# Optimization experiments

Measured on AMD Instinct MI355X. Metric: run time of the kernel, lower is better.

The kernel has to match this reference:

```python
import jax, jax.numpy as jnp
import numpy as np

N_NODES = 100000
NEG_SLOPE = 0.01  # torch F.leaky_relu default


def gcn_conv(x, src, dst, norm, W, b):
    # x: [N, Fin]; src/dst: [E+N] (self-loops included); norm: [E+N]
    h = x @ W                                  # [N, Fout] dense transform
    msg = h[src] * norm[:, None]               # gather + edge-wise scale
    out = jax.ops.segment_sum(msg, dst, num_segments=x.shape[0])  # scatter-add
    return out + b


def build_graph(edge_index, n_nodes):
    # Add self-loops and compute symmetric GCN normalization deg^-1/2 * deg^-1/2
    loop = jnp.arange(n_nodes, dtype=edge_index.dtype)
    src = jnp.concatenate([edge_index[0], loop])
    dst = jnp.concatenate([edge_index[1], loop])
    deg = jax.ops.segment_sum(jnp.ones_like(dst, dtype=jnp.float32), dst,
                              num_segments=n_nodes)
    dinv = jnp.where(deg > 0, jax.lax.rsqrt(deg), 0.0)
    norm = dinv[src] * dinv[dst]
    return src, dst, norm


def setup_inputs() -> dict:
    key = jax.random.key(0)
    ks = jax.random.split(key, 8)
    in_c, out_c = 256, 64
    hid = 2 * out_c
    x = jax.random.normal(ks[0], (N_NODES, in_c), dtype=jnp.float32)
    edge_index = jax.random.randint(ks[1], (2, 1600000), 0, N_NODES, dtype=jnp.int64)
    def glorot(k, fan_in, fan_out):
        s = jnp.sqrt(6.0 / (fan_in + fan_out))
        return jax.random.uniform(k, (fan_in, fan_out), jnp.float32, -s, s)
    return {
        "x": x,
        "edge_index": edge_index,
        "W1": glorot(ks[2], in_c, hid),
        "b1": jnp.zeros((hid,), jnp.float32),
        "Wmu": glorot(ks[3], hid, out_c),
        "bmu": jnp.zeros((out_c,), jnp.float32),
        "Wlv": glorot(ks[4], hid, out_c),
        "blv": jnp.zeros((out_c,), jnp.float32),
    }


def reference(x, edge_index, W1, b1, Wmu, bmu, Wlv, blv):
    src, dst, norm = build_graph(edge_index, x.shape[0])
    h = gcn_conv(x, src, dst, norm, W1, b1)
    h = jnp.where(h >= 0, h, NEG_SLOPE * h)  # leaky_relu
    mu = gcn_conv(h, src, dst, norm, Wmu, bmu)
    logvar = gcn_conv(h, src, dst, norm, Wlv, blv)
    return (mu, logvar)
```

## Files before the change

### kernel.cpp

```cpp
#include <hip/hip_runtime.h>

typedef unsigned short bf16_t;
typedef short s16x8 __attribute__((ext_vector_type(8)));
typedef float f32x4 __attribute__((ext_vector_type(4)));


#define NBKT 782
#define BSH  7
#define BMSK 127
#define CAPS 512

__device__ __forceinline__ float bf2f(unsigned short u) {
    unsigned int v = ((unsigned int)u) << 16;
    float f;
    __builtin_memcpy(&f, &v, 4);
    return f;
}
__device__ __forceinline__ unsigned short f2bf(float f) {
    unsigned int x;
    __builtin_memcpy(&x, &f, 4);
    unsigned int r = x + 0x7fffu + ((x >> 16) & 1u);
    return (unsigned short)(r >> 16);
}
__device__ __forceinline__ unsigned pack2(float a, float b) {
    return (unsigned)f2bf(a) | ((unsigned)f2bf(b) << 16);
}
__device__ __forceinline__ float ldf(const void* p, long long i, unsigned f32) {
    return f32 ? ((const float*)p)[i] : bf2f(((const unsigned short*)p)[i]);
}
__device__ __forceinline__ int ldi(const void* p, long long i, unsigned i64) {
    return i64 ? (int)((const long long*)p)[i] : ((const int*)p)[i];
}
__device__ __forceinline__ s16x8 ld8u(const unsigned short* p) {
    return *(const s16x8*)p;
}
__device__ __forceinline__ f32x4 mfma16(s16x8 a, s16x8 b, f32x4 c) {
    return __builtin_amdgcn_mfma_f32_16x16x32_bf16(a, b, c, 0, 0, 0);
}
__device__ __forceinline__ void cvt_hl(const float* p, s16x8& hi, s16x8& lo) {
    const float4 u = *(const float4*)p;
    const float4 w = *(const float4*)(p + 4);
    float v[8] = {u.x, u.y, u.z, u.w, w.x, w.y, w.z, w.w};
#pragma unroll
    for (int j = 0; j < 8; ++j) {
        unsigned short h = f2bf(v[j]);
        hi[j] = (short)h;
        lo[j] = (short)f2bf(v[j] - bf2f(h));
    }
}

__global__ __launch_bounds__(256) void k_zero(unsigned* __restrict__ p, int n) {
    int i = blockIdx.x * 256 + threadIdx.x;
    if (i < n) p[i] = 0;
}

__global__ __launch_bounds__(256) void k_detect(const void* x, const void* W1,
                                                const void* ei, unsigned* flags) {
    __shared__ float smx[256];
    __shared__ float smw[256];
    __shared__ int   szc[256];
    int tid = threadIdx.x;
    const unsigned short* xu = (const unsigned short*)x;
    float mx = 0.f;
    for (int i = tid; i < 4096; i += 256) {
        unsigned short w = xu[i];
        if ((w & 0x7fffu) >= 0x7f80u) mx = 1e30f;
        else { float f = fabsf(bf2f(w)); if (f > mx) mx = f; }
    }
    smx[tid] = mx;
    const unsigned short* wu = (const unsigned short*)W1;
    float mw = 0.f;
    for (int i = tid; i < 4096; i += 256) {
        unsigned short w = wu[i];
        if ((w & 0x7fffu) >= 0x7f80u) mw = 1e30f;
        else { float f = fabsf(bf2f(w)); if (f > mw) mw = f; }
    }
    smw[tid] = mw;
    const int* eu = (const int*)ei;
    int zc = 0;
    for (int i = tid; i < 128; i += 256)
        if ((i & 1) && eu[i] == 0) ++zc;
    szc[tid] = zc;
    __syncthreads();
    for (int off = 128; off > 0; off >>= 1) {
        if (tid < off) {
            if (smx[tid + off] > smx[tid]) smx[tid] = smx[tid + off];
            if (smw[tid + off] > smw[tid]) smw[tid] = smw[tid + off];
            szc[tid] += szc[tid + off];
        }
        __syncthreads();
    }
    if (tid == 0) {
        flags[0] = (smx[0] > 1e4f) ? 1u : 0u;
        flags[1] = (smw[0] > 10.f) ? 1u : 0u;
        flags[2] = (szc[0] >= 56) ? 1u : 0u;
    }
}

__global__ __launch_bounds__(256) void k_bucket(const void* ei, const unsigned* det,
                                                int* __restrict__ btail,
                                                unsigned* __restrict__ bstore,
                                                int E, int N) {
    int e = blockIdx.x * 256 + threadIdx.x;
    if (e >= E) return;
    unsigned i64 = det[2];
    int s = ldi(ei, e, i64);
    int d = ldi(ei, (long long)E + e, i64);
    if ((unsigned)d >= (unsigned)N) return;
    int b = d >> BSH;
    int sub = blockIdx.x & 7;
    int slot = atomicAdd(&btail[sub * NBKT + b], 1);
    if (slot < CAPS) {
        unsigned src = ((unsigned)s < (unsigned)N) ? (unsigned)s : (unsigned)d;
        bstore[((long long)(b * 8 + sub)) * CAPS + slot] =
            ((unsigned)(d & BMSK) << 24) | src;
    }
}

__global__ __launch_bounds__(256) void k_bhist(const int* __restrict__ btail,
                                               const unsigned* __restrict__ bstore,
                                               int* __restrict__ cnt, int N) {
    __shared__ int lh[128];
    __shared__ int ln[8];
    const int b = blockIdx.x;
    const int tid = threadIdx.x;
    if (tid < 128) lh[tid] = 0;
    if (tid < 8) {
        int t = btail[tid * NBKT + b];
        ln[tid] = t < CAPS ? t : CAPS;
    }
    __syncthreads();
#pragma unroll 1
    for (int s = 0; s < 8; ++s) {
        int n = ln[s];
        const unsigned* base = &bstore[((long long)(b * 8 + s)) * CAPS];
        for (int i = tid; i < n; i += 256)
            atomicAdd(&lh[base[i] >> 24], 1);
    }
    __syncthreads();
    int node = b * 128 + tid;
    if (tid < 128 && node < N) cnt[node] = lh[tid];
}

__global__ __launch_bounds__(256) void k_dinv(const int* __restrict__ cnt,
                                              float* __restrict__ dinv, int N) {
    int i = blockIdx.x * 256 + threadIdx.x;
    if (i < N) dinv[i] = rsqrtf((float)cnt[i] + 1.0f);
}

__global__ __launch_bounds__(256) void k_scan_blk(const int* __restrict__ cnt,
                                                  int* __restrict__ pos,
                                                  int* __restrict__ bsum, int N) {
    __shared__ int sh[256];
    const int tid = threadIdx.x;
    const int base = blockIdx.x * 1024 + tid * 4;
    int v[4];
#pragma unroll
    for (int j = 0; j < 4; ++j) v[j] = (base + j < N) ? cnt[base + j] : 0;
    int s = v[0] + v[1] + v[2] + v[3];
    sh[tid] = s;
    __syncthreads();
    for (int off = 1; off < 256; off <<= 1) {
        int t = (tid >= off) ? sh[tid - off] : 0;
        __syncthreads();
        sh[tid] += t;
        __syncthreads();
    }
    int run = sh[tid] - s;
#pragma unroll
    for (int j = 0; j < 4; ++j) {
        if (base + j < N) pos[base + j] = run;
        run += v[j];
    }
    if (tid == 255) bsum[blockIdx.x] = sh[255];
}

__global__ void k_scan_top(int* __restrict__ bsum, int nb) {
    if (threadIdx.x == 0 && blockIdx.x == 0) {
        int running = 0;
        for (int b = 0; b < nb; ++b) {
            int t = bsum[b];
            bsum[b] = running;
            running += t;
        }
    }
}

__global__ __launch_bounds__(256) void k_scan_add(int* __restrict__ pos,
                                                  const int* __restrict__ bsum, int N) {
    int add = bsum[blockIdx.x];
    int base = blockIdx.x * 1024;
    for (int i = threadIdx.x; i < 1024; i += 256)
        if (base + i < N) pos[base + i] += add;
}

__global__ __launch_bounds__(256) void k_emit(const int* __restrict__ btail,
                                              const unsigned* __restrict__ bstore,
                                              const int* __restrict__ pos,
                                              int* __restrict__ srt, int N) {
    __shared__ int lstart[128];
    __shared__ int loff[128];
    __shared__ int ln[8];
    __shared__ int stage[4096];
    const int b = blockIdx.x;
    const int tid = threadIdx.x;
    const int base0 = pos[b * 128];
    if (tid < 128) {
        int node = b * 128 + tid;
        lstart[tid] = (node < N) ? (pos[node] - base0) : 0;
        loff[tid] = 0;
    }
    if (tid < 8) {
        int t = btail[tid * NBKT + b];
        ln[tid] = t < CAPS ? t : CAPS;
    }
    __syncthreads();
#pragma unroll 1
    for (int s = 0; s < 8; ++s) {
        int n = ln[s];
        const unsigned* bp = &bstore[((long long)(b * 8 + s)) * CAPS];
        for (int i = tid; i < n; i += 256) {
            unsigned rec = bp[i];
            int dl = rec >> 24;
            int slot = atomicAdd(&loff[dl], 1);
            stage[lstart[dl] + slot] = (int)(rec & 0xffffffu);
        }
    }
    __syncthreads();
    int total = ln[0] + ln[1] + ln[2] + ln[3] + ln[4] + ln[5] + ln[6] + ln[7];
    for (int i = tid; i < total; i += 256)
        srt[base0 + i] = stage[i];
}

__global__ __launch_bounds__(256) void k_wsplit(const void* Wa, const void* Wb,
                                                const unsigned* det, int K,
                                                unsigned short* __restrict__ bth,
                                                unsigned short* __restrict__ btl) {
    int idx = blockIdx.x * 256 + threadIdx.x;
    if (idx >= K * 128) return;
    int k = idx >> 7, n = idx & 127;
    unsigned wf = det[1];
    float w;
    if (Wb) w = (n < 64) ? ldf(Wa, (long long)k * 64 + n, wf)
                         : ldf(Wb, (long long)k * 64 + (n - 64), wf);
    else    w = ldf(Wa, idx, wf);
    unsigned short h = f2bf(w);
    bth[(long long)n * K + k] = h;
    btl[(long long)n * K + k] = f2bf(w - bf2f(h));
}

__global__ __launch_bounds__(256, 4) void k_gemm1m(
    const void* __restrict__ x, const unsigned* __restrict__ det,
    const unsigned short* __restrict__ bth,
    const unsigned short* __restrict__ btl,
    const float* __restrict__ dinv,
    unsigned* __restrict__ Cp, int N) {
    const int lane = threadIdx.x & 63;
    const int wid  = threadIdx.x >> 6;
    const int wr = wid >> 1, wc = wid & 1;
    const int l15 = lane & 15, lg = lane >> 4;
    const long long r0 = (long long)blockIdx.x * 64 + wr * 32;
    long long ar[2];
#pragma unroll
    for (int m = 0; m < 2; ++m) {
        long long r = r0 + m * 16 + l15;
        ar[m] = (r < N) ? r : (N - 1);
    }
    int bn[4];
#pragma unroll
    for (int n = 0; n < 4; ++n) bn[n] = wc * 64 + n * 16 + l15;

    f32x4 acc[2][4] = {};
    if (!det[0]) {
        const unsigned short* xp = (const unsigned short*)x;
#pragma unroll 2
        for (int k0 = 0; k0 < 256; k0 += 32) {
            const int kb = k0 + lg * 8;
            s16x8 a[2], bh[4], bl[4];
#pragma unroll
            for (int m = 0; m < 2; ++m) a[m] = ld8u(xp + ar[m] * 256 + kb);
#pragma unroll
            for (int n = 0; n < 4; ++n) {
                bh[n] = ld8u(bth + (long long)bn[n] * 256 + kb);
                bl[n] = ld8u(btl + (long long)bn[n] * 256 + kb);
            }
#pragma unroll
            for (int m = 0; m < 2; ++m)
#pragma unroll
                for (int n = 0; n < 4; ++n) {
                    acc[m][n] = mfma16(a[m], bh[n], acc[m][n]);
                    acc[m][n] = mfma16(a[m], bl[n], acc[m][n]);
                }
        }
    } else {
        const float* xp = (const float*)x;
#pragma unroll 2
        for (int k0 = 0; k0 < 256; k0 += 32) {
            const int kb = k0 + lg * 8;
            s16x8 ah[2], al[2], bh[4], bl[4];
#pragma unroll
            for (int m = 0; m < 2; ++m) cvt_hl(xp + ar[m] * 256 + kb, ah[m], al[m]);
#pragma unroll
            for (int n = 0; n < 4; ++n) {
                bh[n] = ld8u(bth + (long long)bn[n] * 256 + kb);
                bl[n] = ld8u(btl + (long long)bn[n] * 256 + kb);
            }
#pragma unroll
            for (int m = 0; m < 2; ++m)
#pragma unroll
                for (int n = 0; n < 4; ++n) {
                    acc[m][n] = mfma16(ah[m], bh[n], acc[m][n]);
                    acc[m][n] = mfma16(ah[m], bl[n], acc[m][n]);
                    acc[m][n] = mfma16(al[m], bh[n], acc[m][n]);
                }
        }
    }
#pragma unroll
    for (int m = 0; m < 2; ++m)
#pragma unroll
        for (int n = 0; n < 4; ++n) {
            const int col = wc * 64 + n * 16 + l15;
#pragma unroll
            for (int r = 0; r < 4; ++r) {
                long long row = r0 + m * 16 + lg * 4 + r;
                float v = acc[m][n][r] * dinv[(row < N) ? row : (N - 1)];
                float p = __shfl_xor(v, 1);
                if (!(lane & 1) && row < N)
                    Cp[row * 64 + (col >> 1)] = pack2(v, p);
            }
        }
}

__global__ __launch_bounds__(256, 4) void k_gemm2m(
    const unsigned short* __restrict__ hap,
    const unsigned short* __restrict__ bth,
    const unsigned short* __restrict__ btl,
    const void* bmu, const void* blv, const unsigned* __restrict__ det,
    float* __restrict__ outMu, float* __restrict__ outLv, int N) {
    const int lane = threadIdx.x & 63;
    const int wid  = threadIdx.x >> 6;
    const int wr = wid >> 1, wc = wid & 1;
    const int l15 = lane & 15, lg = lane >> 4;
    const long long r0 = (long long)blockIdx.x * 64 + wr * 32;
    long long ar[2];
#pragma unroll
    for (int m = 0; m < 2; ++m) {
        long long r = r0 + m * 16 + l15;
        ar[m] = (r < N) ? r : (N - 1);
    }
    int bn[4];
#pragma unroll
    for (int n = 0; n < 4; ++n) bn[n] = wc * 64 + n * 16 + l15;

    f32x4 acc[2][4] = {};
#pragma unroll
    for (int k0 = 0; k0 < 128; k0 += 32) {
        const int kb = k0 + lg * 8;
        s16x8 a[2], bh[4], bl[4];
#pragma unroll
        for (int m = 0; m < 2; ++m) a[m] = ld8u(hap + ar[m] * 128 + kb);
#pragma unroll
        for (int n = 0; n < 4; ++n) {
            bh[n] = ld8u(bth + (long long)bn[n] * 128 + kb);
            bl[n] = ld8u(btl + (long long)bn[n] * 128 + kb);
        }
#pragma unroll
        for (int m = 0; m < 2; ++m)
#pragma unroll
            for (int n = 0; n < 4; ++n) {
                acc[m][n] = mfma16(a[m], bh[n], acc[m][n]);
                acc[m][n] = mfma16(a[m], bl[n], acc[m][n]);
            }
    }
    __syncthreads();
    const unsigned wf = det[1];
#pragma unroll
    for (int m = 0; m < 2; ++m)
#pragma unroll
        for (int n = 0; n < 4; ++n) {
            const int col = wc * 64 + n * 16 + l15;
            const float bias = (col < 64) ? ldf(bmu, col, wf)
                                          : ldf(blv, col - 64, wf);
#pragma unroll
            for (int r = 0; r < 4; ++r) {
                long long row = r0 + m * 16 + lg * 4 + r;
                if (row < N) {
                    float v = acc[m][n][r] + bias;
                    if (col < 64) outMu[row * 64 + col] = v;
                    else          outLv[row * 64 + (col - 64)] = v;
                }
            }
        }
}

__global__ __launch_bounds__(256) void k_gather(const unsigned* __restrict__ hp,
                                                const int* __restrict__ srt,
                                                const int* __restrict__ cnt,
                                                const int* __restrict__ pos,
                                                const float* __restrict__ dinv,
                                                const void* bias, const unsigned* det,
                                                int leaky, int prescaleOut,
                                                unsigned* __restrict__ outp, int N) {
    int node = blockIdx.x * 4 + (threadIdx.x >> 6);
    if (node >= N) return;
    int lane = threadIdx.x & 63;
    int beg = pos[node];
    int end = beg + cnt[node];
    float dd = dinv[node];
    unsigned hv = hp[(long long)node * 64 + lane];
    float a0 = bf2f((unsigned short)(hv & 0xffffu));
    float a1 = bf2f((unsigned short)(hv >> 16));
    for (int q = beg; q < end; q += 8) {
        int s[8];
        unsigned v[8];
#pragma unroll
        for (int j = 0; j < 8; ++j) {
            int qq = q + j;
            s[j] = srt[(qq < end) ? qq : beg];
        }
#pragma unroll
        for (int j = 0; j < 8; ++j)
            v[j] = hp[(long long)s[j] * 64 + lane];
#pragma unroll
        for (int j = 0; j < 8; ++j) {
            bool on = (q + j) < end;
            a0 += on ? bf2f((unsigned short)(v[j] & 0xffffu)) : 0.f;
            a1 += on ? bf2f((unsigned short)(v[j] >> 16)) : 0.f;
        }
    }
    a0 *= dd;
    a1 *= dd;
    if (bias) {
        a0 += ldf(bias, 2 * lane, det[1]);
        a1 += ldf(bias, 2 * lane + 1, det[1]);
    }
    if (leaky) {
        a0 = (a0 >= 0.f) ? a0 : 0.01f * a0;
        a1 = (a1 >= 0.f) ? a1 : 0.01f * a1;
    }
    if (prescaleOut) { a0 *= dd; a1 *= dd; }
    outp[(long long)node * 64 + lane] = pack2(a0, a1);
}

__global__ void k_sentinel(float* out, long long lvOff) {
    if (threadIdx.x == 0 && blockIdx.x == 0) {
        out[0] = 9.99e5f;
        out[lvOff] = 9.98e5f;
    }
}

extern "C" void kernel_launch(void* const* d_in, const int* in_sizes, int n_in,
                              void* d_out, int out_size, void* d_ws, size_t ws_size,
                              hipStream_t stream) {
    (void)out_size;
    const int N = 100000, E = 1600000;
    bool ok = (n_in == 8) && in_sizes[0] == 25600000 && in_sizes[1] == 3200000 &&
              in_sizes[2] == 32768 && in_sizes[3] == 128 &&
              in_sizes[4] == 8192 && in_sizes[5] == 64 &&
              in_sizes[6] == 8192 && in_sizes[7] == 64 &&
              ws_size >= (size_t)21 * 1024 * 1024;
    if (!ok) {
        k_sentinel<<<1, 64, 0, stream>>>((float*)d_out, (long long)N * 64);
        return;
    }
    const void* x   = d_in[0];
    const void* ei  = d_in[1];
    const void* W1  = d_in[2];
    const void* b1  = d_in[3];
    const void* Wmu = d_in[4];
    const void* bmu = d_in[5];
    const void* Wlv = d_in[6];
    const void* blv = d_in[7];

    char* w = (char*)d_ws;
    auto carve = [&](size_t bytes) {
        char* p = w;
        w += (bytes + 255) & ~(size_t)255;
        return p;
    };
    unsigned* flags = (unsigned*)carve(64);
    int*    cnt  = (int*)carve((size_t)N * 4);
    int*    pos  = (int*)carve((size_t)N * 4);
    float*  dinv = (float*)carve((size_t)N * 4);
    int*    bsum = (int*)carve(4096);
    int*    srt  = (int*)carve((size_t)E * 4);
    unsigned short* bt1h = (unsigned short*)carve(128 * 256 * 2);
    unsigned short* bt1l = (unsigned short*)carve(128 * 256 * 2);
    unsigned short* bt2h = (unsigned short*)carve(128 * 128 * 2);
    unsigned short* bt2l = (unsigned short*)carve(128 * 128 * 2);
    int*      btail  = (int*)carve((size_t)NBKT * 8 * 4);
    unsigned* bstore = (unsigned*)carve((size_t)NBKT * 8 * CAPS * 4);

    float* M = (float*)d_out;
    float* L = M + (size_t)N * 64;
    unsigned* Mp = (unsigned*)M;
    unsigned* Lp = (unsigned*)L;

    const int nb = (N + 1023) / 1024;
    const int gblk = (N + 3) / 4;
    const int gb64 = (N + 63) / 64;

    k_zero<<<1, 64, 0, stream>>>(flags, 16);
    k_detect<<<1, 256, 0, stream>>>(x, W1, ei, flags);
    k_zero<<<(NBKT * 8 + 255) / 256, 256, 0, stream>>>((unsigned*)btail, NBKT * 8);

    k_bucket<<<(E + 255) / 256, 256, 0, stream>>>(ei, flags, btail, bstore, E, N);
    k_bhist<<<NBKT, 256, 0, stream>>>(btail, bstore, cnt, N);
    k_dinv<<<(N + 255) / 256, 256, 0, stream>>>(cnt, dinv, N);
    k_scan_blk<<<nb, 256, 0, stream>>>(cnt, pos, bsum, N);
    k_scan_top<<<1, 64, 0, stream>>>(bsum, nb);
    k_scan_add<<<nb, 256, 0, stream>>>(pos, bsum, N);
    k_emit<<<NBKT, 256, 0, stream>>>(btail, bstore, pos, srt, N);

    k_wsplit<<<(256 * 128 + 255) / 256, 256, 0, stream>>>(W1, nullptr, flags, 256,
                                                          bt1h, bt1l);
    k_wsplit<<<(128 * 128 + 255) / 256, 256, 0, stream>>>(Wmu, Wlv, flags, 128,
                                                          bt2h, bt2l);

    k_gemm1m<<<gb64, 256, 0, stream>>>(x, flags, bt1h, bt1l, dinv, Mp, N);
    k_gather<<<gblk, 256, 0, stream>>>(Mp, srt, cnt, pos, dinv, b1, flags, 1, 1,
                                       Lp, N);
    k_gather<<<gblk, 256, 0, stream>>>(Lp, srt, cnt, pos, dinv, nullptr, flags,
                                       0, 0, Mp, N);
    k_gemm2m<<<gb64, 256, 0, stream>>>((const unsigned short*)Mp, bt2h, bt2l,
                                       bmu, blv, flags, M, L, N);
}
```

Before: 560.4 us.

## Stage GEMM1 tiles in LDS with async global-to-LDS loads and 128-row tiles

Replaces the register-direct first GEMM with a 128x128 block tile whose A and B operands are loaded into shared memory through global_load_lds using an XOR-style swizzle, then read into MFMA fragments. Each wave now computes a 64x64 sub-tile, so each B fragment is reused across more rows. The fp32-input path also drops the lo*lo-free third product ordering, issuing hi/lo products in a different order. The intent is to cut redundant global loads of the weight matrix and raise MFMA density, at the cost of higher LDS use, fewer resident blocks, and barriers with no double buffering.

```diff
diff --git a/kernel.cpp b/kernel.cpp
--- a/kernel.cpp
+++ b/kernel.cpp
@@ -36,6 +36,11 @@
 }
 __device__ __forceinline__ f32x4 mfma16(s16x8 a, s16x8 b, f32x4 c) {
     return __builtin_amdgcn_mfma_f32_16x16x32_bf16(a, b, c, 0, 0, 0);
+}
+__device__ __forceinline__ void gload16(const void* g, void* l) {
+    __builtin_amdgcn_global_load_lds(
+        (const __attribute__((address_space(1))) void*)g,
+        (__attribute__((address_space(3))) void*)l, 16, 0, 0);
 }
 __device__ __forceinline__ void cvt_hl(const float* p, s16x8& hi, s16x8& lo) {
     const float4 u = *(const float4*)p;
@@ -249,84 +254,131 @@
     btl[(long long)n * K + k] = f2bf(w - bf2f(h));
 }
 
-__global__ __launch_bounds__(256, 4) void k_gemm1m(
+__global__ __launch_bounds__(256, 3) void k_gemm1s(
     const void* __restrict__ x, const unsigned* __restrict__ det,
     const unsigned short* __restrict__ bth,
     const unsigned short* __restrict__ btl,
     const float* __restrict__ dinv,
     unsigned* __restrict__ Cp, int N) {
-    const int lane = threadIdx.x & 63;
-    const int wid  = threadIdx.x >> 6;
+    __shared__ unsigned short sA[128 * 64];
+    __shared__ unsigned short sBh[128 * 64];
+    __shared__ unsigned short sBl[128 * 64];
+    const int tid  = threadIdx.x;
+    const int lane = tid & 63;
+    const int wid  = tid >> 6;
     const int wr = wid >> 1, wc = wid & 1;
     const int l15 = lane & 15, lg = lane >> 4;
-    const long long r0 = (long long)blockIdx.x * 64 + wr * 32;
-    long long ar[2];
-#pragma unroll
-    for (int m = 0; m < 2; ++m) {
-        long long r = r0 + m * 16 + l15;
-        ar[m] = (r < N) ? r : (N - 1);
-    }
-    int bn[4];
-#pragma unroll
-    for (int n = 0; n < 4; ++n) bn[n] = wc * 64 + n * 16 + l15;
-
-    f32x4 acc[2][4] = {};
+    const int rowbase = blockIdx.x * 128;
+
+    f32x4 acc[4][4] = {};
+
     if (!det[0]) {
         const unsigned short* xp = (const unsigned short*)x;
-#pragma unroll 2
+        const int sr8 = lane >> 3;
+        const int sp  = lane & 7;
+#pragma unroll 1
+        for (int k0 = 0; k0 < 256; k0 += 64) {
+#pragma unroll
+            for (int q = 0; q < 4; ++q) {
+                int r = wid * 32 + q * 8 + sr8;
+                int grow = rowbase + r;
+                if (grow >= N) grow = N - 1;
+                int c = (sp - r) & 7;
+                gload16(xp + (long long)grow * 256 + k0 + c * 8,
+                        &sA[(wid * 32 + q * 8) * 64]);
+            }
+#pragma unroll
+            for (int q = 0; q < 4; ++q) {
+                int r = wid * 32 + q * 8 + sr8;
+                int c = (sp - r) & 7;
+                long long goff = (long long)r * 256 + k0 + c * 8;
+                gload16(bth + goff, &sBh[(wid * 32 + q * 8) * 64]);
+                gload16(btl + goff, &sBl[(wid * 32 + q * 8) * 64]);
+            }
+            __syncthreads();
+#pragma unroll
+            for (int kk = 0; kk < 2; ++kk) {
+                const int cbase = kk * 4 + lg;
+                s16x8 a[4], b[4];
+#pragma unroll
+                for (int m = 0; m < 4; ++m) {
+                    int lrow = wr * 64 + m * 16 + l15;
+                    int p = (cbase + lrow) & 7;
+                    a[m] = ld8u(&sA[lrow * 64 + p * 8]);
+                }
+#pragma unroll
+                for (int n = 0; n < 4; ++n) {
+                    int lcol = wc * 64 + n * 16 + l15;
+                    int p = (cbase + lcol) & 7;
+                    b[n] = ld8u(&sBh[lcol * 64 + p * 8]);
+                }
+#pragma unroll
+                for (int m = 0; m < 4; ++m)
+#pragma unroll
+                    for (int n = 0; n < 4; ++n)
+                        acc[m][n] = mfma16(a[m], b[n], acc[m][n]);
+#pragma unroll
+                for (int n = 0; n < 4; ++n) {
+                    int lcol = wc * 64 + n * 16 + l15;
+                    int p = (cbase + lcol) & 7;
+                    b[n] = ld8u(&sBl[lcol * 64 + p * 8]);
+                }
+#pragma unroll
+                for (int m = 0; m < 4; ++m)
+#pragma unroll
+                    for (int n = 0; n < 4; ++n)
+                        acc[m][n] = mfma16(a[m], b[n], acc[m][n]);
+            }
+            __syncthreads();
+        }
+    } else {
+        const float* xpf = (const float*)x;
+        long long ar[4];
+#pragma unroll
+        for (int m = 0; m < 4; ++m) {
+            long long r = rowbase + wr * 64 + m * 16 + l15;
+            ar[m] = (r < N) ? r : (N - 1);
+        }
+        int bn[4];
+#pragma unroll
+        for (int n = 0; n < 4; ++n) bn[n] = wc * 64 + n * 16 + l15;
+#pragma unroll 1
         for (int k0 = 0; k0 < 256; k0 += 32) {
             const int kb = k0 + lg * 8;
-            s16x8 a[2], bh[4], bl[4];
-#pragma unroll
-            for (int m = 0; m < 2; ++m) a[m] = ld8u(xp + ar[m] * 256 + kb);
-#pragma unroll
-            for (int n = 0; n < 4; ++n) {
-                bh[n] = ld8u(bth + (long long)bn[n] * 256 + kb);
-                bl[n] = ld8u(btl + (long long)bn[n] * 256 + kb);
-            }
-#pragma unroll
-            for (int m = 0; m < 2; ++m)
+            s16x8 ah[4], al[4], b[4];
+#pragma unroll
+            for (int m = 0; m < 4; ++m) cvt_hl(xpf + ar[m] * 256 + kb, ah[m], al[m]);
+#pragma unroll
+            for (int n = 0; n < 4; ++n) b[n] = ld8u(bth + (long long)bn[n] * 256 + kb);
+#pragma unroll
+            for (int m = 0; m < 4; ++m)
 #pragma unroll
                 for (int n = 0; n < 4; ++n) {
-                    acc[m][n] = mfma16(a[m], bh[n], acc[m][n]);
-                    acc[m][n] = mfma16(a[m], bl[n], acc[m][n]);
+                    acc[m][n] = mfma16(ah[m], b[n], acc[m][n]);
+                    acc[m][n] = mfma16(al[m], b[n], acc[m][n]);
                 }
-        }
-    } else {
-        const float* xp = (const float*)x;
-#pragma unroll 2
-        for (int k0 = 0; k0 < 256; k0 += 32) {
-            const int kb = k0 + lg * 8;
-            s16x8 ah[2], al[2], bh[4], bl[4];
-#pragma unroll
-            for (int m = 0; m < 2; ++m) cvt_hl(xp + ar[m] * 256 + kb, ah[m], al[m]);
-#pragma unroll
-            for (int n = 0; n < 4; ++n) {
-                bh[n] = ld8u(bth + (long long)bn[n] * 256 + kb);
-                bl[n] = ld8u(btl + (long long)bn[n] * 256 + kb);
-            }
-#pragma unroll
-            for (int m = 0; m < 2; ++m)
-#pragma unroll
-                for (int n = 0; n < 4; ++n) {
-                    acc[m][n] = mfma16(ah[m], bh[n], acc[m][n]);
-                    acc[m][n] = mfma16(ah[m], bl[n], acc[m][n]);
-                    acc[m][n] = mfma16(al[m], bh[n], acc[m][n]);
-                }
-        }
-    }
-#pragma unroll
-    for (int m = 0; m < 2; ++m)
+#pragma unroll
+            for (int n = 0; n < 4; ++n) b[n] = ld8u(btl + (long long)bn[n] * 256 + kb);
+#pragma unroll
+            for (int m = 0; m < 4; ++m)
+#pragma unroll
+                for (int n = 0; n < 4; ++n)
+                    acc[m][n] = mfma16(ah[m], b[n], acc[m][n]);
+        }
+    }
+
+#pragma unroll
+    for (int m = 0; m < 4; ++m)
 #pragma unroll
         for (int n = 0; n < 4; ++n) {
             const int col = wc * 64 + n * 16 + l15;
 #pragma unroll
             for (int r = 0; r < 4; ++r) {
-                long long row = r0 + m * 16 + lg * 4 + r;
+                int row = rowbase + wr * 64 + m * 16 + lg * 4 + r;
                 float v = acc[m][n][r] * dinv[(row < N) ? row : (N - 1)];
                 float p = __shfl_xor(v, 1);
                 if (!(lane & 1) && row < N)
-                    Cp[row * 64 + (col >> 1)] = pack2(v, p);
+                    Cp[(long long)row * 64 + (col >> 1)] = pack2(v, p);
             }
         }
 }
@@ -498,7 +550,8 @@
 
     const int nb = (N + 1023) / 1024;
     const int gblk = (N + 3) / 4;
-    const int gb64 = (N + 63) / 64;
+    const int gb64  = (N + 63) / 64;
+    const int gb128 = (N + 127) / 128;
 
     k_zero<<<1, 64, 0, stream>>>(flags, 16);
     k_detect<<<1, 256, 0, stream>>>(x, W1, ei, flags);
@@ -517,7 +570,7 @@
     k_wsplit<<<(128 * 128 + 255) / 256, 256, 0, stream>>>(Wmu, Wlv, flags, 128,
                                                           bt2h, bt2l);
 
-    k_gemm1m<<<gb64, 256, 0, stream>>>(x, flags, bt1h, bt1l, dinv, Mp, N);
+    k_gemm1s<<<gb128, 256, 0, stream>>>(x, flags, bt1h, bt1l, dinv, Mp, N);
     k_gather<<<gblk, 256, 0, stream>>>(Mp, srt, cnt, pos, dinv, b1, flags, 1, 1,
                                        Lp, N);
     k_gather<<<gblk, 256, 0, stream>>>(Lp, srt, cnt, pos, dinv, nullptr, flags,
```

Result: faster. 549.2 us (-2.0%).
